# Optimization experiments

Hardware: AMD Instinct MI355X
Metric: run time of the kernel (lower is better)

## Reference

```python
import jax, jax.numpy as jnp
import numpy as np

EMBED_DIM = 512
KERNEL = 17


def setup_inputs() -> dict:
    key = jax.random.key(0)
    ks = jax.random.split(key, 5)
    B, L, C = 2, 8192, EMBED_DIM
    s = C ** -0.5
    x = jax.random.normal(ks[0], (B, L, C), dtype=jnp.float32)
    # weights stored as (in, out); equivalent to torch Linear weight.T
    w_qkv = jax.random.normal(ks[1], (C, 3 * C), dtype=jnp.float32) * s
    w_width = jax.random.normal(ks[2], (C, 1), dtype=jnp.float32) * s
    b_width = jax.random.normal(ks[3], (1,), dtype=jnp.float32) * 0.01
    w_out = jax.random.normal(ks[4], (C, C), dtype=jnp.float32) * s
    return {"x": x, "w_qkv": w_qkv, "w_width": w_width, "b_width": b_width, "w_out": w_out}


def reference(x, w_qkv, w_width, b_width, w_out):
    B, L, C = x.shape
    K = KERNEL
    half_k = K // 2
    scale = C ** -0.5

    qkv = x @ w_qkv                      # [B,L,3C]
    q, k, v = jnp.split(qkv, 3, axis=-1)

    # learned soft window width in [1, K]
    width = jax.nn.sigmoid(x @ w_width + b_width) * (K - 1) + 1.0   # [B,L,1]

    # sliding windows of k/v: pad along L then gather K-sized windows
    k_pad = jnp.pad(k, ((0, 0), (half_k, half_k), (0, 0)))
    v_pad = jnp.pad(v, ((0, 0), (half_k, half_k), (0, 0)))
    idx = jnp.arange(L)[:, None] + jnp.arange(K)[None, :]           # [L,K]
    k_win = k_pad[:, idx]                # [B,L,K,C]
    v_win = v_pad[:, idx]                # [B,L,K,C]

    scores = jnp.einsum('blc,blkc->blk', q, k_win) * scale          # [B,L,K]

    rel_pos = jnp.abs(jnp.arange(K, dtype=jnp.float32) - half_k)    # [K]
    soft_mask = jax.nn.sigmoid((width - rel_pos) * 5.0)             # [B,L,K]
    scores = scores - (1.0 - soft_mask) * 10000.0

    attn = jax.nn.softmax(scores, axis=-1)
    out = jnp.einsum('blk,blkc->blc', attn, v_win)                  # [B,L,C]
    return (out + v) @ w_out
```

## Files before the change

kernel.cpp:

```cpp
#include <hip/hip_runtime.h>

typedef unsigned short u16;
typedef unsigned int   u32;
typedef __attribute__((ext_vector_type(8))) short          shortx8;
typedef __attribute__((ext_vector_type(8))) unsigned short ushortx8;
typedef __attribute__((ext_vector_type(4))) float          floatx4;

#define AS1 __attribute__((address_space(1)))
#define AS3 __attribute__((address_space(3)))

#define SEG 8208
#define LV  16416

__device__ __forceinline__ float b2f(u16 v) {
  return __uint_as_float(((u32)v) << 16);
}
__device__ __forceinline__ u16 f2b(float f) {
  u32 u = __float_as_uint(f);
  u += 0x7FFF + ((u >> 16) & 1);
  return (u16)(u >> 16);
}
__device__ __forceinline__ void cp16(const void* g, void* l) {
  __builtin_amdgcn_global_load_lds((AS1 u32*)g, (AS3 u32*)l, 16, 0, 0);
}

__global__ void transpose_cast(const float* __restrict__ in, u16* __restrict__ out,
                               int R, int C) {
  __shared__ u16 tile[32][33];
  const int tx = threadIdx.x & 31;
  const int ty = threadIdx.x >> 5;
  const int cb = blockIdx.x * 32;
  const int rb = blockIdx.y * 32;
#pragma unroll
  for (int i = 0; i < 32; i += 8)
    tile[ty + i][tx] = f2b(in[(size_t)(rb + ty + i) * C + cb + tx]);
  __syncthreads();
#pragma unroll
  for (int i = 0; i < 32; i += 8)
    out[(size_t)(cb + ty + i) * R + rb + tx] = tile[tx][ty + i];
}

__global__ __launch_bounds__(256)
void cast_width(const float* __restrict__ x, const float* __restrict__ w_width,
                const float* __restrict__ b_width, u16* __restrict__ xb,
                float* __restrict__ width) {
  const int lane = threadIdx.x & 63;
  const int row  = blockIdx.x * 4 + (threadIdx.x >> 6);
  const float* xp = x + (size_t)row * 512 + lane * 8;
  floatx4 v0 = *(const floatx4*)xp;
  floatx4 v1 = *(const floatx4*)(xp + 4);
  floatx4 w0 = *(const floatx4*)(w_width + lane * 8);
  floatx4 w1 = *(const floatx4*)(w_width + lane * 8 + 4);
  float s = 0.f;
  ushortx8 o;
#pragma unroll
  for (int j = 0; j < 4; ++j) {
    s += v0[j] * w0[j] + v1[j] * w1[j];
    o[j] = f2b(v0[j]); o[4 + j] = f2b(v1[j]);
  }
  *(ushortx8*)(xb + (size_t)row * 512 + lane * 8) = o;
#pragma unroll
  for (int m = 32; m >= 1; m >>= 1) s += __shfl_xor(s, m, 64);
  if (lane == 0)
    width[row] = 16.f / (1.f + __expf(-(s + b_width[0]))) + 1.f;
}

__global__ void vt_zero_pad(u16* __restrict__ Vt) {
  const int idx = blockIdx.x * 256 + threadIdx.x;
  const int ch = idx >> 5;
  const int k  = idx & 31;
  const int seg = k >> 4;
  const int j   = k & 15;
  const int col = seg * SEG + (j < 8 ? j : 8192 + j);
  Vt[(size_t)ch * LV + col] = 0;
}

template <int MODE>
__global__ __launch_bounds__(256, 2)
void gemm_bt(const u16* __restrict__ A, const u16* __restrict__ Bt,
             void* __restrict__ C0, u16* __restrict__ Kb, u16* __restrict__ Vt) {
  const int K = 512;
  __shared__ alignas(16) u16 As[128 * 32];
  __shared__ alignas(16) u16 Bs[128 * 32];
  const int tid  = threadIdx.x;
  const int lane = tid & 63;
  const int wave = tid >> 6;
  const int quad = lane >> 4;
  const int lr   = lane & 15;
  const int row0 = blockIdx.x * 128;
  const int col0 = blockIdx.y * 128;
  const int wr   = (wave >> 1) * 64;
  const int wc   = (wave & 1) * 64;

  floatx4 acc[4][4];
#pragma unroll
  for (int i = 0; i < 4; ++i)
#pragma unroll
    for (int j = 0; j < 4; ++j) acc[i][j] = (floatx4)0.0f;

  const int rr = tid >> 2;
  const int cc = (tid & 3) * 8;
  const u16* a0 = A  + (size_t)(row0 + rr)      * K + cc;
  const u16* a1 = A  + (size_t)(row0 + 64 + rr) * K + cc;
  const u16* b0 = Bt + (size_t)(col0 + rr)      * K + cc;
  const u16* b1 = Bt + (size_t)(col0 + 64 + rr) * K + cc;
  u16* as0 = &As[tid * 8];
  u16* as1 = &As[(256 + tid) * 8];
  u16* bs0 = &Bs[tid * 8];
  u16* bs1 = &Bs[(256 + tid) * 8];

  for (int k0 = 0; k0 < K; k0 += 32) {
    cp16(a0 + k0, as0);
    cp16(a1 + k0, as1);
    cp16(b0 + k0, bs0);
    cp16(b1 + k0, bs1);
    __syncthreads();

    shortx8 af[4], bf[4];
#pragma unroll
    for (int mi = 0; mi < 4; ++mi)
      af[mi] = *(const shortx8*)&As[(wr + mi * 16 + lr) * 32 + quad * 8];
#pragma unroll
    for (int ni = 0; ni < 4; ++ni)
      bf[ni] = *(const shortx8*)&Bs[(wc + ni * 16 + lr) * 32 + quad * 8];
#pragma unroll
    for (int mi = 0; mi < 4; ++mi)
#pragma unroll
      for (int ni = 0; ni < 4; ++ni)
        acc[mi][ni] = __builtin_amdgcn_mfma_f32_16x16x32_bf16(
            af[mi], bf[ni], acc[mi][ni], 0, 0, 0);
    __syncthreads();
  }

  if constexpr (MODE == 1) {
    if (col0 < 1024) {
      u16* dst = (col0 < 512) ? (u16*)C0 : Kb;
      const int cb = col0 & 511;
#pragma unroll
      for (int mi = 0; mi < 4; ++mi)
#pragma unroll
        for (int ni = 0; ni < 4; ++ni)
#pragma unroll
          for (int r = 0; r < 4; ++r) {
            int row = row0 + wr + mi * 16 + quad * 4 + r;
            int col = cb + wc + ni * 16 + lr;
            dst[(size_t)row * 512 + col] = f2b(acc[mi][ni][r]);
          }
    } else {
      const int cb = col0 - 1024;
#pragma unroll
      for (int mi = 0; mi < 4; ++mi)
#pragma unroll
        for (int ni = 0; ni < 4; ++ni)
#pragma unroll
          for (int r = 0; r < 4; ++r) {
            int row = row0 + wr + mi * 16 + quad * 4 + r;
            int ch  = cb + wc + ni * 16 + lr;
            int bb  = row >> 13, pib = row & 8191;
            Vt[(size_t)ch * LV + (size_t)bb * SEG + 8 + pib] = f2b(acc[mi][ni][r]);
          }
    }
  } else {
    float* Cf = (float*)C0;
#pragma unroll
    for (int mi = 0; mi < 4; ++mi)
#pragma unroll
      for (int ni = 0; ni < 4; ++ni)
#pragma unroll
        for (int r = 0; r < 4; ++r) {
          int row = row0 + wr + mi * 16 + quad * 4 + r;
          int col = col0 + wc + ni * 16 + lr;
          Cf[(size_t)row * 512 + col] = acc[mi][ni][r];
        }
  }
}

__global__ __launch_bounds__(256)
void attn_mfma(const u16* __restrict__ Q, const u16* __restrict__ Kb,
               const u16* __restrict__ Vt, const float* __restrict__ width,
               u16* __restrict__ Out) {
  __shared__ float Sp[8][16][16];
  __shared__ u16   P[16][32];
  __shared__ u16   O[4][16][128];
  const int tid  = threadIdx.x;
  const int lane = tid & 63;
  const int wave = tid >> 6;
  const int quad = lane >> 4;
  const int lr   = lane & 15;
  const int p0   = blockIdx.x * 16;
  const int pib0 = p0 & 8191;
  const int bb   = p0 >> 13;

  floatx4 s0 = (floatx4)0.0f, s1 = (floatx4)0.0f;
#pragma unroll
  for (int s = 0; s < 4; ++s) {
    const int k0 = wave * 128 + s * 32 + quad * 8;
    shortx8 af = *(const shortx8*)(Q  + (size_t)(p0 + lr) * 512 + k0);
    shortx8 f0 = *(const shortx8*)(Kb + (ptrdiff_t)(p0 - 8 + lr) * 512 + k0);
    shortx8 f1 = *(const shortx8*)(Kb + (ptrdiff_t)(p0 + 8 + lr) * 512 + k0);
    s0 = __builtin_amdgcn_mfma_f32_16x16x32_bf16(af, f0, s0, 0, 0, 0);
    s1 = __builtin_amdgcn_mfma_f32_16x16x32_bf16(af, f1, s1, 0, 0, 0);
  }
#pragma unroll
  for (int r = 0; r < 4; ++r) {
    Sp[wave * 2 + 0][quad * 4 + r][lr] = s0[r];
    Sp[wave * 2 + 1][quad * 4 + r][lr] = s1[r];
  }
  __syncthreads();

  {
    const int row = tid >> 4, cg = tid & 15;
    const float scale = 0.044194173824159216f;
    const float wrow  = width[p0 + row];
    float sv[2]; float mx = -1e30f;
#pragma unroll
    for (int t = 0; t < 2; ++t) {
      const int col = t * 16 + cg;
      float s = Sp[t][row][cg] + Sp[2 + t][row][cg] +
                Sp[4 + t][row][cg] + Sp[6 + t][row][cg];
      const int d  = col - row;
      const int jb = pib0 + col - 8;
      const bool inband  = (d >= 0) && (d <= 16);
      const bool inbatch = ((unsigned)jb < 8192u);
      float rel  = fabsf((float)(d - 8));
      float mask = 1.f / (1.f + __expf(-5.f * (wrow - rel)));
      float pen  = (1.f - mask) * 10000.f;
      float val  = inband ? ((inbatch ? s * scale : 0.f) - pen) : -1e30f;
      sv[t] = val;
      mx = fmaxf(mx, val);
    }
#pragma unroll
    for (int m = 8; m >= 1; m >>= 1) mx = fmaxf(mx, __shfl_xor(mx, m, 64));
    float e0 = __expf(sv[0] - mx), e1 = __expf(sv[1] - mx);
    float sum = e0 + e1;
#pragma unroll
    for (int m = 8; m >= 1; m >>= 1) sum += __shfl_xor(sum, m, 64);
    const float inv = 1.f / sum;
    P[row][cg]      = f2b(e0 * inv + ((cg - row) == 8 ? 1.f : 0.f));
    P[row][cg + 16] = f2b(e1 * inv + ((cg + 16 - row) == 8 ? 1.f : 0.f));
  }
  __syncthreads();

  shortx8 pf = *(const shortx8*)&P[lr][quad * 8];
  const size_t cb0 = (size_t)bb * SEG + pib0;
#pragma unroll
  for (int ct = 0; ct < 8; ++ct) {
    const int ch = wave * 128 + ct * 16 + lr;
    shortx8 vf = *(const shortx8*)(Vt + (size_t)ch * LV + cb0 + quad * 8);
    floatx4 o = __builtin_amdgcn_mfma_f32_16x16x32_bf16(pf, vf, (floatx4)0.0f,
                                                        0, 0, 0);
#pragma unroll
    for (int r = 0; r < 4; ++r)
      O[wave][quad * 4 + r][ct * 16 + lr] = f2b(o[r]);
  }
  __syncthreads();
  {
    const int orow = lane >> 2;
#pragma unroll
    for (int i = 0; i < 4; ++i) {
      const int c = i * 32 + (lane & 3) * 8;
      ushortx8 v = *(const ushortx8*)&O[wave][orow][c];
      *(ushortx8*)(Out + (size_t)(p0 + orow) * 512 + wave * 128 + c) = v;
    }
  }
}

extern "C" void kernel_launch(void* const* d_in, const int* in_sizes, int n_in,
                              void* d_out, int out_size, void* d_ws, size_t ws_size,
                              hipStream_t stream) {
  const float* x       = (const float*)d_in[0];
  const float* w_qkv   = (const float*)d_in[1];
  const float* w_width = (const float*)d_in[2];
  const float* b_width = (const float*)d_in[3];
  const float* w_out   = (const float*)d_in[4];
  float* out = (float*)d_out;

  const int M = 16384, C = 512, N3 = 1536;
  char* ws = (char*)d_ws;
  u16*   xb    = (u16*)(ws);
  u16*   Qb    = (u16*)(ws + 16777216);
  u16*   Kb    = (u16*)(ws + 33554432 + 8192);
  u16*   Vt    = (u16*)(ws + 50348032);
  u16*   wqkvT = (u16*)(ws + 67158016);
  u16*   woutT = (u16*)(ws + 68730880);
  float* width = (float*)(ws + 69255168);

  dim3 blk(256);
  vt_zero_pad<<<dim3(64), blk, 0, stream>>>(Vt);
  cast_width<<<dim3(M / 4), blk, 0, stream>>>(x, w_width, b_width, xb, width);
  transpose_cast<<<dim3(N3 / 32, C / 32), blk, 0, stream>>>(w_qkv, wqkvT, C, N3);
  transpose_cast<<<dim3(C / 32, C / 32), blk, 0, stream>>>(w_out, woutT, C, C);
  gemm_bt<1><<<dim3(M / 128, N3 / 128), blk, 0, stream>>>(xb, wqkvT, Qb, Kb, Vt);
  attn_mfma<<<dim3(M / 16), blk, 0, stream>>>(Qb, Kb, Vt, width, Qb);
  gemm_bt<2><<<dim3(M / 128, C / 128), blk, 0, stream>>>(Qb, woutT, out, nullptr, nullptr);
}
```

Baseline: 168.2 us.

## Deepen GEMM k-tile to 64 with XOR-swizzled LDS and staged vectorized epilogue

The bf16 GEMM now loads 64-wide k tiles per iteration into LDS using an XOR swizzle on 16-byte chunks, which halves the number of barrier pairs and is meant to avoid LDS bank conflicts on fragment reads. For the QKV mode, accumulators are first written to a padded LDS tile and then stored to global memory as 16-byte vectors. The V^T scatter is transposed through LDS so its stores become contiguous along L instead of strided 2-byte writes. This adds LDS footprint (about 34 KB per block), which could limit occupancy against launch_bounds(256,2), and adds an extra barrier in the epilogue.

New measurement: 160.5 us. 1.05x faster.

```diff
diff --git a/kernel.cpp b/kernel.cpp
--- a/kernel.cpp
+++ b/kernel.cpp
@@ -80,8 +80,9 @@
 void gemm_bt(const u16* __restrict__ A, const u16* __restrict__ Bt,
              void* __restrict__ C0, u16* __restrict__ Kb, u16* __restrict__ Vt) {
   const int K = 512;
-  __shared__ alignas(16) u16 As[128 * 32];
-  __shared__ alignas(16) u16 Bs[128 * 32];
+  __shared__ alignas(16) u16 lds[17408];
+  u16* As = lds;
+  u16* Bs = lds + 8192;
   const int tid  = threadIdx.x;
   const int lane = tid & 63;
   const int wave = tid >> 6;
@@ -98,37 +99,42 @@
 #pragma unroll
     for (int j = 0; j < 4; ++j) acc[i][j] = (floatx4)0.0f;
 
-  const int rr = tid >> 2;
-  const int cc = (tid & 3) * 8;
-  const u16* a0 = A  + (size_t)(row0 + rr)      * K + cc;
-  const u16* a1 = A  + (size_t)(row0 + 64 + rr) * K + cc;
-  const u16* b0 = Bt + (size_t)(col0 + rr)      * K + cc;
-  const u16* b1 = Bt + (size_t)(col0 + 64 + rr) * K + cc;
-  u16* as0 = &As[tid * 8];
-  u16* as1 = &As[(256 + tid) * 8];
-  u16* bs0 = &Bs[tid * 8];
-  u16* bs1 = &Bs[(256 + tid) * 8];
-
-  for (int k0 = 0; k0 < K; k0 += 32) {
-    cp16(a0 + k0, as0);
-    cp16(a1 + k0, as1);
-    cp16(b0 + k0, bs0);
-    cp16(b1 + k0, bs1);
+  int srow[4], scol[4];
+#pragma unroll
+  for (int p = 0; p < 4; ++p) {
+    int c = p * 256 + tid;
+    srow[p] = c >> 3;
+    scol[p] = ((c & 7) ^ (srow[p] & 7)) * 8;
+  }
+  const int swz = lr & 7;
+
+  for (int k0 = 0; k0 < K; k0 += 64) {
+#pragma unroll
+    for (int p = 0; p < 4; ++p)
+      cp16(A + (size_t)(row0 + srow[p]) * K + k0 + scol[p], &As[(p * 256 + tid) * 8]);
+#pragma unroll
+    for (int p = 0; p < 4; ++p)
+      cp16(Bt + (size_t)(col0 + srow[p]) * K + k0 + scol[p], &Bs[(p * 256 + tid) * 8]);
     __syncthreads();
 
-    shortx8 af[4], bf[4];
-#pragma unroll
-    for (int mi = 0; mi < 4; ++mi)
-      af[mi] = *(const shortx8*)&As[(wr + mi * 16 + lr) * 32 + quad * 8];
-#pragma unroll
-    for (int ni = 0; ni < 4; ++ni)
-      bf[ni] = *(const shortx8*)&Bs[(wc + ni * 16 + lr) * 32 + quad * 8];
-#pragma unroll
-    for (int mi = 0; mi < 4; ++mi)
+#pragma unroll
+    for (int ks = 0; ks < 2; ++ks) {
+      shortx8 af[4], bf[4];
+#pragma unroll
+      for (int mi = 0; mi < 4; ++mi)
+        af[mi] = *(const shortx8*)
+            &As[((wr + mi * 16 + lr) * 8 + ((ks * 4 + quad) ^ swz)) * 8];
 #pragma unroll
       for (int ni = 0; ni < 4; ++ni)
-        acc[mi][ni] = __builtin_amdgcn_mfma_f32_16x16x32_bf16(
-            af[mi], bf[ni], acc[mi][ni], 0, 0, 0);
+        bf[ni] = *(const shortx8*)
+            &Bs[((wc + ni * 16 + lr) * 8 + ((ks * 4 + quad) ^ swz)) * 8];
+#pragma unroll
+      for (int mi = 0; mi < 4; ++mi)
+#pragma unroll
+        for (int ni = 0; ni < 4; ++ni)
+          acc[mi][ni] = __builtin_amdgcn_mfma_f32_16x16x32_bf16(
+              af[mi], bf[ni], acc[mi][ni], 0, 0, 0);
+    }
     __syncthreads();
   }
 
@@ -141,24 +147,36 @@
 #pragma unroll
         for (int ni = 0; ni < 4; ++ni)
 #pragma unroll
-          for (int r = 0; r < 4; ++r) {
-            int row = row0 + wr + mi * 16 + quad * 4 + r;
-            int col = cb + wc + ni * 16 + lr;
-            dst[(size_t)row * 512 + col] = f2b(acc[mi][ni][r]);
-          }
+          for (int r = 0; r < 4; ++r)
+            lds[(wr + mi * 16 + quad * 4 + r) * 136 + wc + ni * 16 + lr] =
+                f2b(acc[mi][ni][r]);
+      __syncthreads();
+      const int rr = tid >> 4, cc = (tid & 15) * 8;
+#pragma unroll
+      for (int it = 0; it < 8; ++it) {
+        int row = it * 16 + rr;
+        *(ushortx8*)(dst + (size_t)(row0 + row) * 512 + cb + cc) =
+            *(const ushortx8*)&lds[row * 136 + cc];
+      }
     } else {
       const int cb = col0 - 1024;
+      const int bb = row0 >> 13, pib0 = row0 & 8191;
 #pragma unroll
       for (int mi = 0; mi < 4; ++mi)
 #pragma unroll
         for (int ni = 0; ni < 4; ++ni)
 #pragma unroll
-          for (int r = 0; r < 4; ++r) {
-            int row = row0 + wr + mi * 16 + quad * 4 + r;
-            int ch  = cb + wc + ni * 16 + lr;
-            int bb  = row >> 13, pib = row & 8191;
-            Vt[(size_t)ch * LV + (size_t)bb * SEG + 8 + pib] = f2b(acc[mi][ni][r]);
-          }
+          for (int r = 0; r < 4; ++r)
+            lds[(wc + ni * 16 + lr) * 136 + wr + mi * 16 + quad * 4 + r] =
+                f2b(acc[mi][ni][r]);
+      __syncthreads();
+      const int rr = tid >> 4, cc = (tid & 15) * 8;
+#pragma unroll
+      for (int it = 0; it < 8; ++it) {
+        int chl = it * 16 + rr;
+        ushortx8 v = *(const ushortx8*)&lds[chl * 136 + cc];
+        *(ushortx8*)(Vt + (size_t)(cb + chl) * LV + (size_t)bb * SEG + 8 + pib0 + cc) = v;
+      }
     }
   } else {
     float* Cf = (float*)C0;
```
